# Kernel tuning notes

Hardware: AMD Instinct MI355X
Metric: run time of the kernel (lower is better)

The kernel has to match this reference:

```python
import jax, jax.numpy as jnp
import numpy as np
import math

FACTOR = 1

def setup_inputs() -> dict:
    key = jax.random.key(0)
    k1, k2, k3 = jax.random.split(key, 3)
    B, L, H, E = 32, 1024, 8, 64
    return {
        "queries": jax.random.normal(k1, (B, L, H, E), dtype=jnp.float32),
        "keys": jax.random.normal(k2, (B, L, H, E), dtype=jnp.float32),
        "values": jax.random.normal(k3, (B, L, H, E), dtype=jnp.float32),
        "attn_mask": 0,
    }


def reference(queries, keys, values, attn_mask):
    # queries/keys/values: [B, L, H, E] (S == L so no pad/truncate needed)
    B, L, H, E = queries.shape
    q = jnp.transpose(queries, (0, 2, 3, 1))  # [B,H,E,L]
    k = jnp.transpose(keys, (0, 2, 3, 1))
    v = jnp.transpose(values, (0, 2, 3, 1))   # [B,H,D,L]

    # FFT cross-correlation
    q_fft = jnp.fft.rfft(q, axis=-1)
    k_fft = jnp.fft.rfft(k, axis=-1)
    corr = jnp.fft.irfft(q_fft * jnp.conj(k_fft), n=L, axis=-1)  # [B,H,E,L]

    # top-k delay selection (global over batch, as in source)
    top_k = min(int(FACTOR * math.log(L)), L // 4, 32)  # static: 6
    mean_value = corr.mean(axis=(1, 2))                 # [B,L]
    weights, indices = jax.lax.top_k(mean_value.mean(axis=0), top_k)  # [k]
    tmp_corr = jax.nn.softmax(weights)                  # [k]

    # weighted circular-shift aggregation: roll(v, -indices[i]) summed with tmp_corr[i]
    pos = (jnp.arange(L)[None, :] + indices[:, None]) % L  # [k,L]
    patterns = v[:, :, :, pos]                              # [B,H,D,k,L]
    delays_agg = jnp.einsum('k,bhdkl->bhdl', tmp_corr, patterns)

    return jnp.transpose(delays_agg, (0, 3, 1, 2))  # [B,L,H,D]
```

## Files before the change

### kernel.cpp

```cpp
#include <hip/hip_runtime.h>
#include <math.h>

#define L_SEQ 1024
#define TOPK 6
#define RSTR 36
#define PSTR 1156
#define NFBLK 2048

__device__ constexpr float TW32R[16] = {
  1.f, 0.98078528f, 0.92387953f, 0.83146961f, 0.70710678f, 0.55557023f,
  0.38268343f, 0.19509032f, 0.f, -0.19509032f, -0.38268343f, -0.55557023f,
  -0.70710678f, -0.83146961f, -0.92387953f, -0.98078528f};
__device__ constexpr float TW32I[16] = {
  0.f, -0.19509032f, -0.38268343f, -0.55557023f, -0.70710678f, -0.83146961f,
  -0.92387953f, -0.98078528f, -1.f, -0.98078528f, -0.92387953f, -0.83146961f,
  -0.70710678f, -0.55557023f, -0.38268343f, -0.19509032f};

#define FFTSTAGE(M, H, SH)                                                \
  _Pragma("unroll")                                                       \
  for (int k_ = 0; k_ < 32; k_ += (M)) {                                  \
    _Pragma("unroll")                                                     \
    for (int t_ = 0; t_ < (H); ++t_) {                                    \
      const int a_ = k_ + t_, b_ = a_ + (H);                              \
      const int m_ = t_ << (SH);                                          \
      float vr_, vi_;                                                     \
      if (m_ == 0)      { vr_ = zr[b_]; vi_ = zi[b_]; }                   \
      else if (m_ == 8) { vr_ = zi[b_]; vi_ = -zr[b_]; }                  \
      else {                                                              \
        vr_ = zr[b_] * TW32R[m_] - zi[b_] * TW32I[m_];                    \
        vi_ = zr[b_] * TW32I[m_] + zi[b_] * TW32R[m_];                    \
      }                                                                   \
      zr[b_] = zr[a_] - vr_; zi[b_] = zi[a_] - vi_;                       \
      zr[a_] += vr_;         zi[a_] += vi_;                               \
    }                                                                     \
  }

__global__ __launch_bounds__(256, 2) void fft_spec_kernel(
    const float* __restrict__ q, const float* __restrict__ k,
    float* __restrict__ partial)
{
  __shared__ float pr[8 * PSTR];
  __shared__ float pim[8 * PSTR];

  const int tid = threadIdx.x;
  const int bid = blockIdx.x;

  const int wq  = bid >> 3;
  const int xcd = bid & 7;
  const int octet = (wq & 1) | (((wq >> 1) & 3) << 1);
  const int h = (wq >> 3) & 7;
  const int b = (xcd << 2) | (wq >> 6);

  const float* qb = q + (size_t)b * 524288 + h * 64 + octet * 8;
  const float* kb = k + (size_t)b * 524288 + h * 64 + octet * 8;

  {
    const int ep = (tid & 1) * 4;
    const int lb = tid >> 1;
    const int r  = lb & 31;
    const int cb = lb >> 5;
    #pragma unroll
    for (int it = 0; it < 8; ++it) {
      const int l = it * 128 + lb;
      const float4 qv = *(const float4*)(qb + (size_t)l * 512 + ep);
      const float4 kv = *(const float4*)(kb + (size_t)l * 512 + ep);
      const int w = r * RSTR + cb + it * 4;
      pr [(ep + 0) * PSTR + w] = qv.x;
      pr [(ep + 1) * PSTR + w] = qv.y;
      pr [(ep + 2) * PSTR + w] = qv.z;
      pr [(ep + 3) * PSTR + w] = qv.w;
      pim[(ep + 0) * PSTR + w] = kv.x;
      pim[(ep + 1) * PSTR + w] = kv.y;
      pim[(ep + 2) * PSTR + w] = kv.z;
      pim[(ep + 3) * PSTR + w] = kv.w;
    }
  }
  __syncthreads();

  const int s = tid >> 5;
  const int i = tid & 31;
  constexpr int BR[32] = {0,16,8,24,4,20,12,28,2,18,10,26,6,22,14,30,
                          1,17,9,25,5,21,13,29,3,19,11,27,7,23,15,31};
  const float astep = (float)i * 6.13592315e-03f;
  float zr[32], zi[32];

  {
    const int rowbase = s * PSTR + i * RSTR;
    float lr[32], li[32];
    #pragma unroll
    for (int m = 0; m < 8; ++m) {
      const float4 vr = *(const float4*)(pr  + rowbase + m * 4);
      const float4 vi = *(const float4*)(pim + rowbase + m * 4);
      lr[m*4+0] = vr.x; lr[m*4+1] = vr.y; lr[m*4+2] = vr.z; lr[m*4+3] = vr.w;
      li[m*4+0] = vi.x; li[m*4+1] = vi.y; li[m*4+2] = vi.z; li[m*4+3] = vi.w;
    }
    #pragma unroll
    for (int p = 0; p < 32; ++p) { zr[p] = lr[BR[p]]; zi[p] = li[BR[p]]; }

    FFTSTAGE(2, 1, 4) FFTSTAGE(4, 2, 3) FFTSTAGE(8, 4, 2)
    FFTSTAGE(16, 8, 1) FFTSTAGE(32, 16, 0)

    #pragma unroll
    for (int k2 = 1; k2 < 32; ++k2) {
      float sa, ca;
      __sincosf(astep * (float)k2, &sa, &ca);
      const float nr = zr[k2] * ca + zi[k2] * sa;
      const float ni = zi[k2] * ca - zr[k2] * sa;
      zr[k2] = nr; zi[k2] = ni;
    }
    #pragma unroll
    for (int m = 0; m < 8; ++m) {
      *(float4*)(pr  + rowbase + m * 4) =
          make_float4(zr[m*4], zr[m*4+1], zr[m*4+2], zr[m*4+3]);
      *(float4*)(pim + rowbase + m * 4) =
          make_float4(zi[m*4], zi[m*4+1], zi[m*4+2], zi[m*4+3]);
    }
  }
  __syncthreads();

  const int j = i;
  {
    float lr[32], li[32];
    #pragma unroll
    for (int r = 0; r < 32; ++r) {
      lr[r] = pr [s * PSTR + r * RSTR + j];
      li[r] = pim[s * PSTR + r * RSTR + j];
    }
    #pragma unroll
    for (int p = 0; p < 32; ++p) { zr[p] = lr[BR[p]]; zi[p] = li[BR[p]]; }
  }
  __syncthreads();

  FFTSTAGE(2, 1, 4) FFTSTAGE(4, 2, 3) FFTSTAGE(8, 4, 2)
  FFTSTAGE(16, 8, 1) FFTSTAGE(32, 16, 0)

  {
    const int t64 = tid & 63;
    const int pl = (t64 & 32) | ((32 - j) & 31);
    const int prow = s * PSTR + j * RSTR;
    float sr_[16], si_[16];

    #pragma unroll
    for (int k1 = 0; k1 < 16; ++k1) {
      float xr = __shfl(zr[31 - k1], pl, 64);
      float xi = __shfl(zi[31 - k1], pl, 64);
      if (j == 0) { xr = zr[(32 - k1) & 31]; xi = zi[(32 - k1) & 31]; }
      const float ar = zr[k1], ai = zi[k1];
      sr_[k1] = 0.5f  * (ar * xi + ai * xr);
      si_[k1] = 0.25f * (ar * ar + ai * ai - xr * xr - xi * xi);
    }
    #pragma unroll
    for (int m = 0; m < 4; ++m) {
      *(float4*)(pr  + prow + m * 4) =
          make_float4(sr_[m*4], sr_[m*4+1], sr_[m*4+2], sr_[m*4+3]);
      *(float4*)(pim + prow + m * 4) =
          make_float4(si_[m*4], si_[m*4+1], si_[m*4+2], si_[m*4+3]);
    }

    #pragma unroll
    for (int k1 = 16; k1 < 32; ++k1) {
      float xr = __shfl(zr[31 - k1], pl, 64);
      float xi = __shfl(zi[31 - k1], pl, 64);
      if (j == 0) { xr = zr[(32 - k1) & 31]; xi = zi[(32 - k1) & 31]; }
      const float ar = zr[k1], ai = zi[k1];
      sr_[k1 - 16] = 0.5f  * (ar * xi + ai * xr);
      si_[k1 - 16] = 0.25f * (ar * ar + ai * ai - xr * xr - xi * xi);
    }
    #pragma unroll
    for (int m = 0; m < 4; ++m) {
      *(float4*)(pr  + prow + 16 + m * 4) =
          make_float4(sr_[m*4], sr_[m*4+1], sr_[m*4+2], sr_[m*4+3]);
      *(float4*)(pim + prow + 16 + m * 4) =
          make_float4(si_[m*4], si_[m*4+1], si_[m*4+2], si_[m*4+3]);
    }
  }
  __syncthreads();

  {
    const int jj = tid >> 3;
    const int kq = tid & 7;
    float arx = 0.f, ary = 0.f, arz = 0.f, arw = 0.f;
    float aix = 0.f, aiy = 0.f, aiz = 0.f, aiw = 0.f;
    #pragma unroll
    for (int s2 = 0; s2 < 8; ++s2) {
      const float4 vr = *(const float4*)(pr  + s2 * PSTR + jj * RSTR + kq * 4);
      const float4 vi = *(const float4*)(pim + s2 * PSTR + jj * RSTR + kq * 4);
      arx += vr.x; ary += vr.y; arz += vr.z; arw += vr.w;
      aix += vi.x; aiy += vi.y; aiz += vi.z; aiw += vi.w;
    }
    const int v = jj * 32 + kq * 4;
    *(float4*)(partial + (size_t)bid * 2048 + v) =
        make_float4(arx, ary, arz, arw);
    *(float4*)(partial + (size_t)bid * 2048 + 1024 + v) =
        make_float4(aix, aiy, aiz, aiw);
  }
}

__global__ __launch_bounds__(256) void spec_reduce(
    const float* __restrict__ partial, float* __restrict__ S4)
{
  const int t = threadIdx.x;
  const int b64 = t & 63, rq = t >> 6;
  const int vb = (blockIdx.x & 31) * 64;
  const int rc = blockIdx.x >> 5;
  const int v = vb + b64;
  float acc = 0.f;
  const int r0 = rc * 512 + rq * 128;
  for (int rr = r0; rr < r0 + 128; ++rr)
    acc += partial[(size_t)rr * 2048 + v];
  __shared__ float sm[4][65];
  sm[rq][b64] = acc;
  __syncthreads();
  if (t < 64)
    S4[(size_t)rc * 2048 + vb + t] =
        sm[0][t] + sm[1][t] + sm[2][t] + sm[3][t];
}

__global__ __launch_bounds__(256) void corr_kernel(
    const float* __restrict__ S4, float* __restrict__ c)
{
  __shared__ float Sr[2048];
  __shared__ float sm[8][33];
  const int t = threadIdx.x;
  #pragma unroll
  for (int u = 0; u < 8; ++u) {
    const int v = u * 256 + t;
    Sr[v] = S4[v] + S4[2048 + v] + S4[4096 + v] + S4[6144 + v];
  }
  __syncthreads();

  const int tau = blockIdx.x * 32 + (t & 31);
  const int jc = t >> 5;
  float acc = 0.f;
  #pragma unroll 4
  for (int jj = 0; jj < 128; ++jj) {
    const int v = jc * 128 + jj;
    const int jt = ((v & 31) << 5) | (v >> 5);
    float s_, c_;
    __sincosf((float)((jt * tau) & 1023) * 6.13592315e-03f, &s_, &c_);
    acc += Sr[v] * c_ - Sr[1024 + v] * s_;
  }
  sm[jc][t & 31] = acc;
  __syncthreads();
  if (t < 32) {
    float r = 0.f;
    #pragma unroll
    for (int g = 0; g < 8; ++g) r += sm[g][t];
    c[blockIdx.x * 32 + t] = r * (1.0f / 16777216.0f);
  }
}

__global__ __launch_bounds__(256) void topk_kernel(
    const float* __restrict__ c, int* __restrict__ idx_out,
    float* __restrict__ w_out)
{
  __shared__ float vals[L_SEQ];
  __shared__ float rv[256];
  __shared__ int ri[256];
  __shared__ float topv[TOPK];
  __shared__ int topi[TOPK];
  const int tid = threadIdx.x;
  for (int i = tid; i < L_SEQ; i += 256) vals[i] = c[i];
  __syncthreads();

  for (int kk = 0; kk < TOPK; ++kk) {
    float bv = -INFINITY;
    int bi = 1 << 30;
    for (int i = tid; i < L_SEQ; i += 256) {
      const float v = vals[i];
      if (v > bv || (v == bv && i < bi)) { bv = v; bi = i; }
    }
    rv[tid] = bv; ri[tid] = bi;
    __syncthreads();
    for (int off = 128; off > 0; off >>= 1) {
      if (tid < off) {
        const float v2 = rv[tid + off];
        const int i2 = ri[tid + off];
        if (v2 > rv[tid] || (v2 == rv[tid] && i2 < ri[tid])) {
          rv[tid] = v2; ri[tid] = i2;
        }
      }
      __syncthreads();
    }
    if (tid == 0) {
      topv[kk] = rv[0];
      topi[kk] = ri[0];
      vals[ri[0]] = -INFINITY;
    }
    __syncthreads();
  }

  if (tid == 0) {
    const float m = topv[0];
    float e[TOPK], sum = 0.f;
    for (int i = 0; i < TOPK; ++i) { e[i] = expf(topv[i] - m); sum += e[i]; }
    const float inv = 1.0f / sum;
    for (int i = 0; i < TOPK; ++i) { w_out[i] = e[i] * inv; idx_out[i] = topi[i]; }
  }
}

__global__ __launch_bounds__(256) void agg_kernel(
    const float* __restrict__ v, const int* __restrict__ idx,
    const float* __restrict__ w, float4* __restrict__ out)
{
  __shared__ int sidx[TOPK];
  __shared__ float sw[TOPK];
  if (threadIdx.x < TOPK) {
    sidx[threadIdx.x] = idx[threadIdx.x];
    sw[threadIdx.x] = w[threadIdx.x];
  }
  __syncthreads();

  const int i = blockIdx.x * 256 + threadIdx.x;
  const int he4 = i & 127;
  const int l = (i >> 7) & (L_SEQ - 1);
  const int b = i >> 17;
  const float4* vb = (const float4*)v + (size_t)b * (L_SEQ * 128);

  float4 acc = make_float4(0.f, 0.f, 0.f, 0.f);
  #pragma unroll
  for (int kk = 0; kk < TOPK; ++kk) {
    const int src = (l + sidx[kk]) & (L_SEQ - 1);
    const float4 vv = vb[(size_t)src * 128 + he4];
    const float wk = sw[kk];
    acc.x += wk * vv.x; acc.y += wk * vv.y;
    acc.z += wk * vv.z; acc.w += wk * vv.w;
  }
  out[i] = acc;
}

extern "C" void kernel_launch(void* const* d_in, const int* in_sizes, int n_in,
                              void* d_out, int out_size, void* d_ws, size_t ws_size,
                              hipStream_t stream) {
  const float* q = (const float*)d_in[0];
  const float* k = (const float*)d_in[1];
  const float* v = (const float*)d_in[2];

  float* out = (float*)d_out;
  float* partial = out;
  float* S4 = out + (size_t)8388608;

  float* c    = (float*)d_ws;
  int*   idxp = (int*)((char*)d_ws + 4096);
  float* wp   = (float*)((char*)d_ws + 4096 + 64);

  fft_spec_kernel<<<NFBLK, 256, 0, stream>>>(q, k, partial);
  spec_reduce<<<128, 256, 0, stream>>>(partial, S4);
  corr_kernel<<<32, 256, 0, stream>>>(S4, c);
  topk_kernel<<<1, 256, 0, stream>>>(c, idxp, wp);
  agg_kernel<<<(L_SEQ * 32 * 128) / 256, 256, 0, stream>>>(v, idxp, wp,
                                                           (float4*)out);
}
```

Baseline: 135.5 us.

## Load q/k tiles directly into LDS via global_load_lds and restructure FFT staging

```diff
diff --git a/kernel.cpp b/kernel.cpp
--- a/kernel.cpp
+++ b/kernel.cpp
@@ -3,6 +3,7 @@
 
 #define L_SEQ 1024
 #define TOPK 6
+#define ROWA 260
 #define RSTR 36
 #define PSTR 1156
 #define NFBLK 2048
@@ -35,15 +36,22 @@
     }                                                                     \
   }
 
+__device__ __forceinline__ void gload_lds16(const float* g, char* l) {
+  __builtin_amdgcn_global_load_lds(
+      (const __attribute__((address_space(1))) void*)g,
+      (__attribute__((address_space(3))) void*)l, 16, 0, 0);
+}
+
 __global__ __launch_bounds__(256, 2) void fft_spec_kernel(
     const float* __restrict__ q, const float* __restrict__ k,
     float* __restrict__ partial)
 {
-  __shared__ float pr[8 * PSTR];
-  __shared__ float pim[8 * PSTR];
+  __shared__ float smem[18496];
 
   const int tid = threadIdx.x;
   const int bid = blockIdx.x;
+  const int lane = tid & 63;
+  const int wid  = tid >> 6;
 
   const int wq  = bid >> 3;
   const int xcd = bid & 7;
@@ -51,28 +59,18 @@
   const int h = (wq >> 3) & 7;
   const int b = (xcd << 2) | (wq >> 6);
 
-  const float* qb = q + (size_t)b * 524288 + h * 64 + octet * 8;
-  const float* kb = k + (size_t)b * 524288 + h * 64 + octet * 8;
-
   {
-    const int ep = (tid & 1) * 4;
-    const int lb = tid >> 1;
-    const int r  = lb & 31;
-    const int cb = lb >> 5;
-    #pragma unroll
-    for (int it = 0; it < 8; ++it) {
-      const int l = it * 128 + lb;
-      const float4 qv = *(const float4*)(qb + (size_t)l * 512 + ep);
-      const float4 kv = *(const float4*)(kb + (size_t)l * 512 + ep);
-      const int w = r * RSTR + cb + it * 4;
-      pr [(ep + 0) * PSTR + w] = qv.x;
-      pr [(ep + 1) * PSTR + w] = qv.y;
-      pr [(ep + 2) * PSTR + w] = qv.z;
-      pr [(ep + 3) * PSTR + w] = qv.w;
-      pim[(ep + 0) * PSTR + w] = kv.x;
-      pim[(ep + 1) * PSTR + w] = kv.y;
-      pim[(ep + 2) * PSTR + w] = kv.z;
-      pim[(ep + 3) * PSTR + w] = kv.w;
+    const size_t sbase = (size_t)b * 524288 + h * 64 + octet * 8
+                       + (size_t)(lane >> 1) * 16384 + (lane & 1) * 4;
+    const float* srcq = q + sbase;
+    const float* srck = k + sbase;
+    char* lq = (char*)smem;
+    char* lk = (char*)smem + 33280;
+    #pragma unroll
+    for (int r8 = 0; r8 < 8; ++r8) {
+      const int row = wid * 8 + r8;
+      gload_lds16(srcq + (size_t)row * 512, lq + row * 1040);
+      gload_lds16(srck + (size_t)row * 512, lk + row * 1040);
     }
   }
   __syncthreads();
@@ -85,21 +83,14 @@
   float zr[32], zi[32];
 
   {
-    const int rowbase = s * PSTR + i * RSTR;
-    float lr[32], li[32];
-    #pragma unroll
-    for (int m = 0; m < 8; ++m) {
-      const float4 vr = *(const float4*)(pr  + rowbase + m * 4);
-      const float4 vi = *(const float4*)(pim + rowbase + m * 4);
-      lr[m*4+0] = vr.x; lr[m*4+1] = vr.y; lr[m*4+2] = vr.z; lr[m*4+3] = vr.w;
-      li[m*4+0] = vi.x; li[m*4+1] = vi.y; li[m*4+2] = vi.z; li[m*4+3] = vi.w;
-    }
-    #pragma unroll
-    for (int p = 0; p < 32; ++p) { zr[p] = lr[BR[p]]; zi[p] = li[BR[p]]; }
-
+    const int basea = i * ROWA;
+    #pragma unroll
+    for (int c = 0; c < 32; ++c) {
+      zr[BR[c]] = smem[basea + c * 8 + s];
+      zi[BR[c]] = smem[8320 + basea + c * 8 + s];
+    }
     FFTSTAGE(2, 1, 4) FFTSTAGE(4, 2, 3) FFTSTAGE(8, 4, 2)
     FFTSTAGE(16, 8, 1) FFTSTAGE(32, 16, 0)
-
     #pragma unroll
     for (int k2 = 1; k2 < 32; ++k2) {
       float sa, ca;
@@ -108,36 +99,33 @@
       const float ni = zi[k2] * ca - zr[k2] * sa;
       zr[k2] = nr; zi[k2] = ni;
     }
-    #pragma unroll
-    for (int m = 0; m < 8; ++m) {
-      *(float4*)(pr  + rowbase + m * 4) =
-          make_float4(zr[m*4], zr[m*4+1], zr[m*4+2], zr[m*4+3]);
-      *(float4*)(pim + rowbase + m * 4) =
-          make_float4(zi[m*4], zi[m*4+1], zi[m*4+2], zi[m*4+3]);
-    }
+  }
+  __syncthreads();
+
+  #pragma unroll
+  for (int k2 = 0; k2 < 32; ++k2) {
+    smem[s * PSTR + k2 * RSTR + i]        = zr[k2];
+    smem[9248 + s * PSTR + k2 * RSTR + i] = zi[k2];
   }
   __syncthreads();
 
   const int j = i;
-  {
-    float lr[32], li[32];
-    #pragma unroll
-    for (int r = 0; r < 32; ++r) {
-      lr[r] = pr [s * PSTR + r * RSTR + j];
-      li[r] = pim[s * PSTR + r * RSTR + j];
-    }
-    #pragma unroll
-    for (int p = 0; p < 32; ++p) { zr[p] = lr[BR[p]]; zi[p] = li[BR[p]]; }
-  }
-  __syncthreads();
-
+  const int rowb = s * PSTR + j * RSTR;
+  #pragma unroll
+  for (int m = 0; m < 8; ++m) {
+    const float4 vr = *(const float4*)(smem + rowb + m * 4);
+    const float4 vi = *(const float4*)(smem + 9248 + rowb + m * 4);
+    zr[BR[4*m+0]] = vr.x; zr[BR[4*m+1]] = vr.y;
+    zr[BR[4*m+2]] = vr.z; zr[BR[4*m+3]] = vr.w;
+    zi[BR[4*m+0]] = vi.x; zi[BR[4*m+1]] = vi.y;
+    zi[BR[4*m+2]] = vi.z; zi[BR[4*m+3]] = vi.w;
+  }
   FFTSTAGE(2, 1, 4) FFTSTAGE(4, 2, 3) FFTSTAGE(8, 4, 2)
   FFTSTAGE(16, 8, 1) FFTSTAGE(32, 16, 0)
 
   {
     const int t64 = tid & 63;
     const int pl = (t64 & 32) | ((32 - j) & 31);
-    const int prow = s * PSTR + j * RSTR;
     float sr_[16], si_[16];
 
     #pragma unroll
@@ -151,9 +139,9 @@
     }
     #pragma unroll
     for (int m = 0; m < 4; ++m) {
-      *(float4*)(pr  + prow + m * 4) =
+      *(float4*)(smem + rowb + m * 4) =
           make_float4(sr_[m*4], sr_[m*4+1], sr_[m*4+2], sr_[m*4+3]);
-      *(float4*)(pim + prow + m * 4) =
+      *(float4*)(smem + 9248 + rowb + m * 4) =
           make_float4(si_[m*4], si_[m*4+1], si_[m*4+2], si_[m*4+3]);
     }
 
@@ -168,9 +156,9 @@
     }
     #pragma unroll
     for (int m = 0; m < 4; ++m) {
-      *(float4*)(pr  + prow + 16 + m * 4) =
+      *(float4*)(smem + rowb + 16 + m * 4) =
           make_float4(sr_[m*4], sr_[m*4+1], sr_[m*4+2], sr_[m*4+3]);
-      *(float4*)(pim + prow + 16 + m * 4) =
+      *(float4*)(smem + 9248 + rowb + 16 + m * 4) =
           make_float4(si_[m*4], si_[m*4+1], si_[m*4+2], si_[m*4+3]);
     }
   }
@@ -183,8 +171,8 @@
     float aix = 0.f, aiy = 0.f, aiz = 0.f, aiw = 0.f;
     #pragma unroll
     for (int s2 = 0; s2 < 8; ++s2) {
-      const float4 vr = *(const float4*)(pr  + s2 * PSTR + jj * RSTR + kq * 4);
-      const float4 vi = *(const float4*)(pim + s2 * PSTR + jj * RSTR + kq * 4);
+      const float4 vr = *(const float4*)(smem + s2 * PSTR + jj * RSTR + kq * 4);
+      const float4 vi = *(const float4*)(smem + 9248 + s2 * PSTR + jj * RSTR + kq * 4);
       arx += vr.x; ary += vr.y; arz += vr.z; arw += vr.w;
       aix += vi.x; aiy += vi.y; aiz += vi.z; aiw += vi.w;
     }
```

New measurement: 139.1 us. 2.6% more time.

## Shrink FFT kernel shared memory to one padded buffer with staged transposes

Applied to the files above, without the earlier changes.

```diff
diff --git a/kernel.cpp b/kernel.cpp
--- a/kernel.cpp
+++ b/kernel.cpp
@@ -3,8 +3,7 @@
 
 #define L_SEQ 1024
 #define TOPK 6
-#define RSTR 36
-#define PSTR 1156
+#define SSTR 1057
 #define NFBLK 2048
 
 __device__ constexpr float TW32R[16] = {
@@ -39,8 +38,7 @@
     const float* __restrict__ q, const float* __restrict__ k,
     float* __restrict__ partial)
 {
-  __shared__ float pr[8 * PSTR];
-  __shared__ float pim[8 * PSTR];
+  __shared__ float smem[8 * SSTR];
 
   const int tid = threadIdx.x;
   const int bid = blockIdx.x;
@@ -54,26 +52,25 @@
   const float* qb = q + (size_t)b * 524288 + h * 64 + octet * 8;
   const float* kb = k + (size_t)b * 524288 + h * 64 + octet * 8;
 
-  {
-    const int ep = (tid & 1) * 4;
-    const int lb = tid >> 1;
-    const int r  = lb & 31;
-    const int cb = lb >> 5;
-    #pragma unroll
-    for (int it = 0; it < 8; ++it) {
-      const int l = it * 128 + lb;
-      const float4 qv = *(const float4*)(qb + (size_t)l * 512 + ep);
-      const float4 kv = *(const float4*)(kb + (size_t)l * 512 + ep);
-      const int w = r * RSTR + cb + it * 4;
-      pr [(ep + 0) * PSTR + w] = qv.x;
-      pr [(ep + 1) * PSTR + w] = qv.y;
-      pr [(ep + 2) * PSTR + w] = qv.z;
-      pr [(ep + 3) * PSTR + w] = qv.w;
-      pim[(ep + 0) * PSTR + w] = kv.x;
-      pim[(ep + 1) * PSTR + w] = kv.y;
-      pim[(ep + 2) * PSTR + w] = kv.z;
-      pim[(ep + 3) * PSTR + w] = kv.w;
-    }
+  const int ep = (tid & 1) * 4;
+  const int lb = tid >> 1;
+  float4 qv[8], kv[8];
+  int colv[8];
+  #pragma unroll
+  for (int it = 0; it < 8; ++it) {
+    const int l = it * 128 + lb;
+    qv[it] = *(const float4*)(qb + (size_t)l * 512 + ep);
+    kv[it] = *(const float4*)(kb + (size_t)l * 512 + ep);
+    colv[it] = (l & 31) * 33 + (l >> 5);
+  }
+
+  #pragma unroll
+  for (int it = 0; it < 8; ++it) {
+    const int col = colv[it];
+    smem[(ep + 0) * SSTR + col] = qv[it].x;
+    smem[(ep + 1) * SSTR + col] = qv[it].y;
+    smem[(ep + 2) * SSTR + col] = qv[it].z;
+    smem[(ep + 3) * SSTR + col] = qv[it].w;
   }
   __syncthreads();
 
@@ -82,117 +79,108 @@
   constexpr int BR[32] = {0,16,8,24,4,20,12,28,2,18,10,26,6,22,14,30,
                           1,17,9,25,5,21,13,29,3,19,11,27,7,23,15,31};
   const float astep = (float)i * 6.13592315e-03f;
+  const int rowbase = s * SSTR + i * 33;
   float zr[32], zi[32];
 
-  {
-    const int rowbase = s * PSTR + i * RSTR;
-    float lr[32], li[32];
-    #pragma unroll
-    for (int m = 0; m < 8; ++m) {
-      const float4 vr = *(const float4*)(pr  + rowbase + m * 4);
-      const float4 vi = *(const float4*)(pim + rowbase + m * 4);
-      lr[m*4+0] = vr.x; lr[m*4+1] = vr.y; lr[m*4+2] = vr.z; lr[m*4+3] = vr.w;
-      li[m*4+0] = vi.x; li[m*4+1] = vi.y; li[m*4+2] = vi.z; li[m*4+3] = vi.w;
-    }
-    #pragma unroll
-    for (int p = 0; p < 32; ++p) { zr[p] = lr[BR[p]]; zi[p] = li[BR[p]]; }
-
-    FFTSTAGE(2, 1, 4) FFTSTAGE(4, 2, 3) FFTSTAGE(8, 4, 2)
-    FFTSTAGE(16, 8, 1) FFTSTAGE(32, 16, 0)
-
-    #pragma unroll
-    for (int k2 = 1; k2 < 32; ++k2) {
-      float sa, ca;
-      __sincosf(astep * (float)k2, &sa, &ca);
-      const float nr = zr[k2] * ca + zi[k2] * sa;
-      const float ni = zi[k2] * ca - zr[k2] * sa;
-      zr[k2] = nr; zi[k2] = ni;
-    }
-    #pragma unroll
-    for (int m = 0; m < 8; ++m) {
-      *(float4*)(pr  + rowbase + m * 4) =
-          make_float4(zr[m*4], zr[m*4+1], zr[m*4+2], zr[m*4+3]);
-      *(float4*)(pim + rowbase + m * 4) =
-          make_float4(zi[m*4], zi[m*4+1], zi[m*4+2], zi[m*4+3]);
-    }
-  }
-  __syncthreads();
-
-  const int j = i;
-  {
-    float lr[32], li[32];
-    #pragma unroll
-    for (int r = 0; r < 32; ++r) {
-      lr[r] = pr [s * PSTR + r * RSTR + j];
-      li[r] = pim[s * PSTR + r * RSTR + j];
-    }
-    #pragma unroll
-    for (int p = 0; p < 32; ++p) { zr[p] = lr[BR[p]]; zi[p] = li[BR[p]]; }
-  }
+  #pragma unroll
+  for (int c = 0; c < 32; ++c) zr[BR[c]] = smem[rowbase + c];
+  __syncthreads();
+
+  #pragma unroll
+  for (int it = 0; it < 8; ++it) {
+    const int col = colv[it];
+    smem[(ep + 0) * SSTR + col] = kv[it].x;
+    smem[(ep + 1) * SSTR + col] = kv[it].y;
+    smem[(ep + 2) * SSTR + col] = kv[it].z;
+    smem[(ep + 3) * SSTR + col] = kv[it].w;
+  }
+  __syncthreads();
+  #pragma unroll
+  for (int c = 0; c < 32; ++c) zi[BR[c]] = smem[rowbase + c];
   __syncthreads();
 
   FFTSTAGE(2, 1, 4) FFTSTAGE(4, 2, 3) FFTSTAGE(8, 4, 2)
   FFTSTAGE(16, 8, 1) FFTSTAGE(32, 16, 0)
-
+  #pragma unroll
+  for (int k2 = 1; k2 < 32; ++k2) {
+    float sa, ca;
+    __sincosf(astep * (float)k2, &sa, &ca);
+    const float nr = zr[k2] * ca + zi[k2] * sa;
+    const float ni = zi[k2] * ca - zr[k2] * sa;
+    zr[k2] = nr; zi[k2] = ni;
+  }
+
+  const int j = i;
+  #pragma unroll
+  for (int k2 = 0; k2 < 32; ++k2) smem[rowbase + k2] = zr[k2];
+  __syncthreads();
+  #pragma unroll
+  for (int c = 0; c < 32; ++c) zr[c] = smem[s * SSTR + BR[c] * 33 + j];
+  __syncthreads();
+  #pragma unroll
+  for (int k2 = 0; k2 < 32; ++k2) smem[rowbase + k2] = zi[k2];
+  __syncthreads();
+  #pragma unroll
+  for (int c = 0; c < 32; ++c) zi[c] = smem[s * SSTR + BR[c] * 33 + j];
+  __syncthreads();
+
+  FFTSTAGE(2, 1, 4) FFTSTAGE(4, 2, 3) FFTSTAGE(8, 4, 2)
+  FFTSTAGE(16, 8, 1) FFTSTAGE(32, 16, 0)
+
+  const int t64 = tid & 63;
+  const int pl = (t64 & 32) | ((32 - j) & 31);
+  const int rowS = s * SSTR + j * 33;
+  float si_all[32];
+
+  #pragma unroll
+  for (int k1 = 0; k1 < 16; ++k1) {
+    float xr = __shfl(zr[31 - k1], pl, 64);
+    float xi = __shfl(zi[31 - k1], pl, 64);
+    if (j == 0) { xr = zr[(32 - k1) & 31]; xi = zi[(32 - k1) & 31]; }
+    const float ar = zr[k1], ai = zi[k1];
+    smem[rowS + k1] = 0.5f  * (ar * xi + ai * xr);
+    si_all[k1]      = 0.25f * (ar * ar + ai * ai - xr * xr - xi * xi);
+  }
+  #pragma unroll
+  for (int k1 = 16; k1 < 32; ++k1) {
+    float xr = __shfl(zr[31 - k1], pl, 64);
+    float xi = __shfl(zi[31 - k1], pl, 64);
+    if (j == 0) { xr = zr[(32 - k1) & 31]; xi = zi[(32 - k1) & 31]; }
+    const float ar = zr[k1], ai = zi[k1];
+    smem[rowS + k1] = 0.5f  * (ar * xi + ai * xr);
+    si_all[k1]      = 0.25f * (ar * ar + ai * ai - xr * xr - xi * xi);
+  }
+  __syncthreads();
+
+  const int jj = tid >> 3;
+  const int kq = tid & 7;
+  const int v = jj * 32 + kq * 4;
   {
-    const int t64 = tid & 63;
-    const int pl = (t64 & 32) | ((32 - j) & 31);
-    const int prow = s * PSTR + j * RSTR;
-    float sr_[16], si_[16];
-
+    float ar4[4] = {0.f, 0.f, 0.f, 0.f};
     #pragma unroll
-    for (int k1 = 0; k1 < 16; ++k1) {
-      float xr = __shfl(zr[31 - k1], pl, 64);
-      float xi = __shfl(zi[31 - k1], pl, 64);
-      if (j == 0) { xr = zr[(32 - k1) & 31]; xi = zi[(32 - k1) & 31]; }
-      const float ar = zr[k1], ai = zi[k1];
-      sr_[k1] = 0.5f  * (ar * xi + ai * xr);
-      si_[k1] = 0.25f * (ar * ar + ai * ai - xr * xr - xi * xi);
-    }
+    for (int pp = 0; pp < 8; ++pp) {
+      const int base = pp * SSTR + jj * 33 + kq * 4;
+      #pragma unroll
+      for (int m = 0; m < 4; ++m) ar4[m] += smem[base + m];
+    }
+    *(float4*)(partial + (size_t)bid * 2048 + v) =
+        make_float4(ar4[0], ar4[1], ar4[2], ar4[3]);
+  }
+  __syncthreads();
+
+  #pragma unroll
+  for (int k1 = 0; k1 < 32; ++k1) smem[rowS + k1] = si_all[k1];
+  __syncthreads();
+  {
+    float ai4[4] = {0.f, 0.f, 0.f, 0.f};
     #pragma unroll
-    for (int m = 0; m < 4; ++m) {
-      *(float4*)(pr  + prow + m * 4) =
-          make_float4(sr_[m*4], sr_[m*4+1], sr_[m*4+2], sr_[m*4+3]);
-      *(float4*)(pim + prow + m * 4) =
-          make_float4(si_[m*4], si_[m*4+1], si_[m*4+2], si_[m*4+3]);
-    }
-
-    #pragma unroll
-    for (int k1 = 16; k1 < 32; ++k1) {
-      float xr = __shfl(zr[31 - k1], pl, 64);
-      float xi = __shfl(zi[31 - k1], pl, 64);
-      if (j == 0) { xr = zr[(32 - k1) & 31]; xi = zi[(32 - k1) & 31]; }
-      const float ar = zr[k1], ai = zi[k1];
-      sr_[k1 - 16] = 0.5f  * (ar * xi + ai * xr);
-      si_[k1 - 16] = 0.25f * (ar * ar + ai * ai - xr * xr - xi * xi);
-    }
-    #pragma unroll
-    for (int m = 0; m < 4; ++m) {
-      *(float4*)(pr  + prow + 16 + m * 4) =
-          make_float4(sr_[m*4], sr_[m*4+1], sr_[m*4+2], sr_[m*4+3]);
-      *(float4*)(pim + prow + 16 + m * 4) =
-          make_float4(si_[m*4], si_[m*4+1], si_[m*4+2], si_[m*4+3]);
-    }
-  }
-  __syncthreads();
-
-  {
-    const int jj = tid >> 3;
-    const int kq = tid & 7;
-    float arx = 0.f, ary = 0.f, arz = 0.f, arw = 0.f;
-    float aix = 0.f, aiy = 0.f, aiz = 0.f, aiw = 0.f;
-    #pragma unroll
-    for (int s2 = 0; s2 < 8; ++s2) {
-      const float4 vr = *(const float4*)(pr  + s2 * PSTR + jj * RSTR + kq * 4);
-      const float4 vi = *(const float4*)(pim + s2 * PSTR + jj * RSTR + kq * 4);
-      arx += vr.x; ary += vr.y; arz += vr.z; arw += vr.w;
-      aix += vi.x; aiy += vi.y; aiz += vi.z; aiw += vi.w;
-    }
-    const int v = jj * 32 + kq * 4;
-    *(float4*)(partial + (size_t)bid * 2048 + v) =
-        make_float4(arx, ary, arz, arw);
+    for (int pp = 0; pp < 8; ++pp) {
+      const int base = pp * SSTR + jj * 33 + kq * 4;
+      #pragma unroll
+      for (int m = 0; m < 4; ++m) ai4[m] += smem[base + m];
+    }
     *(float4*)(partial + (size_t)bid * 2048 + 1024 + v) =
-        make_float4(aix, aiy, aiz, aiw);
+        make_float4(ai4[0], ai4[1], ai4[2], ai4[3]);
   }
 }
 
```

Result: faster. 131.4 us (-3.0%).
